# Optimization experiments

Hardware: AMD Instinct MI355X
Metric: run time of the kernel (lower is better)

## Reference

```python
import jax, jax.numpy as jnp
import numpy as np

B, T, D = 2, 2048, 1024
F = 4096
E = 8


def setup_inputs() -> dict:
    key = jax.random.key(0)
    k0, k1, k2, k3 = jax.random.split(key, 4)
    x = jax.random.normal(k0, (B, T, D), dtype=jnp.float32)
    Wg = jax.random.normal(k1, (E, D), dtype=jnp.float32) * 0.02   # gate Linear weight [E, D]
    W1 = jax.random.normal(k2, (E, D, F), dtype=jnp.float32) * 0.02  # expert up-proj
    W2 = jax.random.normal(k3, (E, F, D), dtype=jnp.float32) * 0.02  # expert down-proj
    return {"x": x, "Wg": Wg, "W1": W1, "W2": W2}


def reference(x, Wg, W1, W2):
    b, t, d = x.shape
    h = x.reshape(-1, d)                              # [N, D], N = b*t
    # --- top-2 gate ---
    logits = h @ Wg.T                                 # [N, E]
    scores, idx = jax.lax.top_k(logits, 2)            # [N, 2], [N, 2]
    scores = jax.nn.softmax(scores.astype(jnp.float32), axis=-1).astype(x.dtype)
    # --- all-expert dense FFN (SiLU MLP) ---
    up = jnp.einsum('nd,edf->enf', h, W1)             # [E, N, F]
    act = jax.nn.silu(up)
    out = jnp.einsum('enf,efd->ned', act, W2)         # [N, E, D]
    # --- combine top-2 ---
    sel = jnp.take_along_axis(out, idx[:, :, None], axis=1)  # [N, 2, D]
    y = jnp.sum(scores[:, :, None] * sel, axis=1)     # [N, D]
    return y.reshape(b, t, d)
```

## Files before the change

### kernel.cpp

```cpp
#include <hip/hip_runtime.h>
#include <hip/hip_bf16.h>
#include <stdint.h>

#define N_TOK 4096
#define D_DIM 1024
#define F_DIM 4096
#define E_NUM 8

typedef unsigned short u16;
typedef __attribute__((ext_vector_type(8))) short short8;
typedef __attribute__((ext_vector_type(4))) float f32x4;

__device__ __forceinline__ u16 f2bf(float f) {
  union { float f; uint32_t u; } v; v.f = f;
  uint32_t u = v.u;
  uint32_t r = (u + 0x7FFFu + ((u >> 16) & 1u)) >> 16;
  return (u16)r;
}

__device__ __forceinline__ void gld_lds16(const u16* g, u16* l) {
  __builtin_amdgcn_global_load_lds(
      (const __attribute__((address_space(1))) uint32_t*)g,
      (__attribute__((address_space(3))) uint32_t*)l, 16, 0, 0);
}

__global__ __launch_bounds__(256) void prep_kernel(
    const float* __restrict__ x, const float* __restrict__ Wg,
    const float* __restrict__ W1,
    u16* __restrict__ xb, int2* __restrict__ choice, float* __restrict__ sc2,
    u16* __restrict__ w1t) {
  int bid = blockIdx.x;
  if (bid < 1024) {
    int n = bid * 4 + (threadIdx.x >> 6);
    int l = threadIdx.x & 63;
    const float* xr = x + (size_t)n * D_DIM;
    u16* xbr = xb + (size_t)n * D_DIM;
    float acc[E_NUM];
#pragma unroll
    for (int e = 0; e < E_NUM; ++e) acc[e] = 0.f;
    for (int d = l; d < D_DIM; d += 64) {
      float xv = xr[d];
      xbr[d] = f2bf(xv);
#pragma unroll
      for (int e = 0; e < E_NUM; ++e) acc[e] += xv * Wg[e * D_DIM + d];
    }
#pragma unroll
    for (int e = 0; e < E_NUM; ++e) {
      float v = acc[e];
#pragma unroll
      for (int off = 32; off > 0; off >>= 1) v += __shfl_xor(v, off);
      acc[e] = v;
    }
    if (l == 0) {
      int i0 = 0; float m0 = acc[0];
#pragma unroll
      for (int e = 1; e < E_NUM; ++e) if (acc[e] > m0) { m0 = acc[e]; i0 = e; }
      int i1 = -1; float m1 = -INFINITY;
#pragma unroll
      for (int e = 0; e < E_NUM; ++e) if (e != i0 && acc[e] > m1) { m1 = acc[e]; i1 = e; }
      float z = __expf(m1 - m0);
      float s0 = 1.f / (1.f + z);
      sc2[n * 2 + 0] = s0;
      sc2[n * 2 + 1] = 1.f - s0;
      choice[n] = make_int2(i0, i1);
    }
    return;
  }
  __shared__ u16 tile[64][72];
  int s = bid - 1024;
  int bx = s & 63, by = (s >> 6) & 15, e = s >> 10;
  const int R = D_DIM, C = F_DIM;
  const float* src = W1 + (size_t)e * R * C;
  u16* dst = w1t + (size_t)e * R * C;
  int r0 = by * 64, c0 = bx * 64;
  int tid = threadIdx.x;
  int lr = tid & 15;
  int rr = tid >> 4;
#pragma unroll
  for (int p = 0; p < 4; ++p) {
    int r = rr + p * 16;
    float4 v = *(const float4*)&src[(size_t)(r0 + r) * C + c0 + lr * 4];
    tile[lr * 4 + 0][r] = f2bf(v.x);
    tile[lr * 4 + 1][r] = f2bf(v.y);
    tile[lr * 4 + 2][r] = f2bf(v.z);
    tile[lr * 4 + 3][r] = f2bf(v.w);
  }
  __syncthreads();
#pragma unroll
  for (int p = 0; p < 4; ++p) {
    int c = rr + p * 16;
    ushort4 o = *(const ushort4*)&tile[c][lr * 4];
    *(ushort4*)&dst[(size_t)(c0 + c) * R + r0 + lr * 4] = o;
  }
}

__global__ void route_kernel(const int2* __restrict__ choice, int* __restrict__ cnt,
                             int* __restrict__ tok_list) {
  int e = blockIdx.x;
  int l = threadIdx.x;
  unsigned long long below = (l == 0) ? 0ull : ((~0ull) >> (64 - l));
  int c = 0;
  for (int it = 0; it < N_TOK / 64; ++it) {
    int n = it * 64 + l;
    int2 ch = choice[n];
    unsigned long long b0 = __ballot(ch.x == e);
    if (ch.x == e) tok_list[e * N_TOK + c + __popcll(b0 & below)] = 2 * n;
    c += __popcll(b0);
    unsigned long long b1 = __ballot(ch.y == e);
    if (ch.y == e) tok_list[e * N_TOK + c + __popcll(b1 & below)] = 2 * n + 1;
    c += __popcll(b1);
  }
  if (l == 0) cnt[e] = c;
}

__global__ void prefix_kernel(const int* __restrict__ cnt, int* __restrict__ base) {
  if (threadIdx.x == 0) {
    int s = 0;
    for (int e = 0; e < E_NUM; ++e) { base[e] = s; s += cnt[e]; }
  }
}

__global__ __launch_bounds__(512) void up_gemm(
    const u16* __restrict__ xb, const u16* __restrict__ w1t,
    const float* __restrict__ W2, u16* __restrict__ w2t,
    const int* __restrict__ cnt, const int* __restrict__ base,
    const int* __restrict__ tok_list, u16* __restrict__ act) {
  __shared__ u16 smem[16384];

  const int bid = blockIdx.x;
  if (bid < 4096) {
    u16 (*tile)[72] = (u16(*)[72])smem;
    int s = bid;
    int bx = s & 7, by = (s >> 3) & 63, e = s >> 9;
    const int R = F_DIM, C = D_DIM;
    const float* src = W2 + (size_t)e * R * C;
    u16* dst = w2t + (size_t)e * R * C;
    int r0 = by * 64, c0 = bx * 128;
    int tid = threadIdx.x;
    {
      int sc = tid & 31, sr = tid >> 5;
      const float* b0p = &src[(size_t)(r0 + sr * 4) * C + c0 + sc * 4];
      float4 v0 = *(const float4*)(b0p + 0 * C);
      float4 v1 = *(const float4*)(b0p + 1 * C);
      float4 v2 = *(const float4*)(b0p + 2 * C);
      float4 v3 = *(const float4*)(b0p + 3 * C);
      ushort4 w;
      w.x = f2bf(v0.x); w.y = f2bf(v1.x); w.z = f2bf(v2.x); w.w = f2bf(v3.x);
      *(ushort4*)&tile[sc * 4 + 0][sr * 4] = w;
      w.x = f2bf(v0.y); w.y = f2bf(v1.y); w.z = f2bf(v2.y); w.w = f2bf(v3.y);
      *(ushort4*)&tile[sc * 4 + 1][sr * 4] = w;
      w.x = f2bf(v0.z); w.y = f2bf(v1.z); w.z = f2bf(v2.z); w.w = f2bf(v3.z);
      *(ushort4*)&tile[sc * 4 + 2][sr * 4] = w;
      w.x = f2bf(v0.w); w.y = f2bf(v1.w); w.z = f2bf(v2.w); w.w = f2bf(v3.w);
      *(ushort4*)&tile[sc * 4 + 3][sr * 4] = w;
    }
    __syncthreads();
    {
      int c = tid >> 2, rq = tid & 3;
      u16* dp = &dst[(size_t)(c0 + c) * R + r0 + rq * 16];
      const u16* tp = &tile[c][rq * 16];
      uint4 a0 = *(const uint4*)(tp + 0);
      uint4 a1 = *(const uint4*)(tp + 8);
      *(uint4*)(dp + 0) = a0;
      *(uint4*)(dp + 8) = a1;
    }
    return;
  }

  u16 (*As)[4096] = (u16(*)[4096])smem;
  u16 (*Bs)[4096] = (u16(*)[4096])(smem + 8192);

  const int ubid = bid - 4096;
  const int orig = (ubid & 7) * 1024 + (ubid >> 3);
  const int bx = orig & 31, by = (orig >> 5) & 31, e = orig >> 10;

  const int ce = cnt[e];
  const int row0 = by * 128;
  if (row0 >= ce) return;
  const int col0 = bx * 128;
  const int be = base[e];

  const int tid = threadIdx.x;
  const int wave = tid >> 6, lane = tid & 63;
  const int wm = wave >> 2, wn = wave & 3;
  const int lr = lane & 15, kq = lane >> 4;

  const int rsA = wave * 16 + (lane >> 2);
  const int kb = (((lane & 3) ^ ((lane >> 3) & 3)) * 8);
  const int kq8 = ((kq ^ ((lr >> 1) & 3)) * 8);

  int ga = row0 + rsA;
  int e0 = (ga < ce) ? (tok_list[e * N_TOK + ga] & (2 * N_TOK - 1)) : 0;
  const u16* srcA = xb + (e0 >> 1) * D_DIM + kb;
  const u16* srcB = w1t + (size_t)(e * F_DIM + col0 + rsA) * D_DIM + kb;

  f32x4 acc[4][2];
#pragma unroll
  for (int m = 0; m < 4; ++m)
#pragma unroll
    for (int n = 0; n < 2; ++n) acc[m][n] = (f32x4){0.f, 0.f, 0.f, 0.f};

#define USTAGE(k0, b)                              \
  do {                                             \
    gld_lds16(srcA + (k0), &As[b][wave * 512]);    \
    gld_lds16(srcB + (k0), &Bs[b][wave * 512]);    \
  } while (0)

#define UCOMPUTE(b)                                                           \
  do {                                                                        \
    short8 a[4], bb[2];                                                       \
    _Pragma("unroll") for (int m = 0; m < 4; ++m)                             \
        a[m] = *(const short8*)&As[b][(wm * 64 + m * 16 + lr) * 32 + kq8];    \
    _Pragma("unroll") for (int n = 0; n < 2; ++n)                             \
        bb[n] = *(const short8*)&Bs[b][(wn * 32 + n * 16 + lr) * 32 + kq8];   \
    _Pragma("unroll") for (int m = 0; m < 4; ++m)                             \
        _Pragma("unroll") for (int n = 0; n < 2; ++n)                         \
            acc[m][n] = __builtin_amdgcn_mfma_f32_16x16x32_bf16(a[m], bb[n], acc[m][n], 0, 0, 0); \
  } while (0)

  const int NT = D_DIM / 32;
  USTAGE(0, 0);
  USTAGE(32, 1);
  asm volatile("s_waitcnt vmcnt(2)" ::: "memory");
  __builtin_amdgcn_s_barrier();
  __builtin_amdgcn_sched_barrier(0);
  int cur = 0;
  for (int t = 0; t < NT; ++t) {
    UCOMPUTE(cur);
    __builtin_amdgcn_sched_barrier(0);
    __builtin_amdgcn_s_barrier();
    __builtin_amdgcn_sched_barrier(0);
    if (t + 2 < NT) {
      USTAGE((t + 2) * 32, cur);
      asm volatile("s_waitcnt vmcnt(2)" ::: "memory");
    } else {
      asm volatile("s_waitcnt vmcnt(0)" ::: "memory");
    }
    __builtin_amdgcn_s_barrier();
    __builtin_amdgcn_sched_barrier(0);
    cur ^= 1;
  }
#undef USTAGE
#undef UCOMPUTE

#pragma unroll
  for (int m = 0; m < 4; ++m) {
#pragma unroll
    for (int rg = 0; rg < 4; ++rg) {
      int row = wm * 64 + m * 16 + kq * 4 + rg;
      int i = row0 + row;
      if (i < ce) {
        u16* dst = act + (size_t)(be + i) * F_DIM + col0 + wn * 32;
#pragma unroll
        for (int n = 0; n < 2; ++n) {
          float v = acc[m][n][rg];
          float s = v / (1.f + __expf(-v));
          dst[n * 16 + lr] = f2bf(s);
        }
      }
    }
  }
}

__global__ __launch_bounds__(512) void down_gemm(
    const u16* __restrict__ act, const u16* __restrict__ w2t,
    const int* __restrict__ cnt, const int* __restrict__ base,
    const int* __restrict__ tok_list, const float* __restrict__ sc2,
    float* __restrict__ out) {
  __shared__ u16 As[2][128 * 32];
  __shared__ u16 Bs[2][128 * 32];
  __shared__ int toks[128];

  const int bid = blockIdx.x;
  const int orig = (bid & 7) * 256 + (bid >> 3);
  const int bx = orig & 7, by = (orig >> 3) & 31, e = orig >> 8;

  const int ce = cnt[e];
  const int row0 = by * 128;
  if (row0 >= ce) return;
  const int col0 = bx * 128;
  const int be = base[e];

  const int tid = threadIdx.x;
  const int wave = tid >> 6, lane = tid & 63;
  const int wm = wave >> 2, wn = wave & 3;
  const int lr = lane & 15, kq = lane >> 4;

  if (tid < 128) {
    int i = row0 + tid;
    toks[tid] = (i < ce) ? tok_list[e * N_TOK + i] : -1;
  }
  __syncthreads();

  const int rsA = wave * 16 + (lane >> 2);
  const int kb = (((lane & 3) ^ ((lane >> 3) & 3)) * 8);
  const int kq8 = ((kq ^ ((lr >> 1) & 3)) * 8);

  int ra = min(be + row0 + rsA, 2 * N_TOK - 1);
  const u16* srcA = act + (size_t)ra * F_DIM + kb;
  const u16* srcB = w2t + (size_t)(e * D_DIM + col0 + rsA) * F_DIM + kb;

  f32x4 acc[4][2];
#pragma unroll
  for (int m = 0; m < 4; ++m)
#pragma unroll
    for (int n = 0; n < 2; ++n) acc[m][n] = (f32x4){0.f, 0.f, 0.f, 0.f};

#define DSTAGE(k0, b)                              \
  do {                                             \
    gld_lds16(srcA + (k0), &As[b][wave * 512]);    \
    gld_lds16(srcB + (k0), &Bs[b][wave * 512]);    \
  } while (0)

#define DCOMPUTE(b)                                                           \
  do {                                                                        \
    short8 a[4], bb[2];                                                       \
    _Pragma("unroll") for (int m = 0; m < 4; ++m)                             \
        a[m] = *(const short8*)&As[b][(wm * 64 + m * 16 + lr) * 32 + kq8];    \
    _Pragma("unroll") for (int n = 0; n < 2; ++n)                             \
        bb[n] = *(const short8*)&Bs[b][(wn * 32 + n * 16 + lr) * 32 + kq8];   \
    _Pragma("unroll") for (int m = 0; m < 4; ++m)                             \
        _Pragma("unroll") for (int n = 0; n < 2; ++n)                         \
            acc[m][n] = __builtin_amdgcn_mfma_f32_16x16x32_bf16(a[m], bb[n], acc[m][n], 0, 0, 0); \
  } while (0)

  const int NT = F_DIM / 32;
  DSTAGE(0, 0);
  DSTAGE(32, 1);
  asm volatile("s_waitcnt vmcnt(2)" ::: "memory");
  __builtin_amdgcn_s_barrier();
  __builtin_amdgcn_sched_barrier(0);
  int cur = 0;
  for (int t = 0; t < NT; ++t) {
    DCOMPUTE(cur);
    __builtin_amdgcn_sched_barrier(0);
    __builtin_amdgcn_s_barrier();
    __builtin_amdgcn_sched_barrier(0);
    if (t + 2 < NT) {
      DSTAGE((t + 2) * 32, cur);
      asm volatile("s_waitcnt vmcnt(2)" ::: "memory");
    } else {
      asm volatile("s_waitcnt vmcnt(0)" ::: "memory");
    }
    __builtin_amdgcn_s_barrier();
    __builtin_amdgcn_sched_barrier(0);
    cur ^= 1;
  }
#undef DSTAGE
#undef DCOMPUTE

#pragma unroll
  for (int m = 0; m < 4; ++m) {
#pragma unroll
    for (int rg = 0; rg < 4; ++rg) {
      int row = wm * 64 + m * 16 + kq * 4 + rg;
      int ent = toks[row];
      if (ent >= 0) {
        int tokn = ent >> 1;
        float sc = sc2[tokn * 2 + (ent & 1)];
        float* dst = out + (size_t)tokn * D_DIM + col0 + wn * 32;
#pragma unroll
        for (int n = 0; n < 2; ++n)
          atomicAdd(&dst[n * 16 + lr], acc[m][n][rg] * sc);
      }
    }
  }
}

extern "C" void kernel_launch(void* const* d_in, const int* in_sizes, int n_in,
                              void* d_out, int out_size, void* d_ws, size_t ws_size,
                              hipStream_t stream) {
  const float* x  = (const float*)d_in[0];
  const float* Wg = (const float*)d_in[1];
  const float* W1 = (const float*)d_in[2];
  const float* W2 = (const float*)d_in[3];
  float* out = (float*)d_out;

  char* ws = (char*)d_ws;
  size_t off = 0;
  u16* xb  = (u16*)(ws + off); off += (size_t)N_TOK * D_DIM * 2;
  u16* w1t = (u16*)(ws + off); off += (size_t)E_NUM * F_DIM * D_DIM * 2;
  u16* w2t = (u16*)(ws + off); off += (size_t)E_NUM * D_DIM * F_DIM * 2;
  u16* act = (u16*)(ws + off); off += (size_t)2 * N_TOK * F_DIM * 2;
  int* tok_list = (int*)(ws + off); off += (size_t)E_NUM * N_TOK * 4;
  float* sc2 = (float*)(ws + off); off += (size_t)N_TOK * 2 * 4;
  int2* choice = (int2*)(ws + off); off += (size_t)N_TOK * 8;
  int* cnt  = (int*)(ws + off); off += 128;
  int* base = (int*)(ws + off); off += 128;

  hipMemsetAsync(d_out, 0, (size_t)out_size * 4, stream);

  prep_kernel<<<dim3(1024 + 8192), 256, 0, stream>>>(x, Wg, W1, xb, choice,
                                                     sc2, w1t);
  route_kernel<<<E_NUM, 64, 0, stream>>>(choice, cnt, tok_list);
  prefix_kernel<<<1, 1, 0, stream>>>(cnt, base);

  up_gemm<<<dim3(4096 + 8192), 512, 0, stream>>>(xb, w1t, W2, w2t, cnt, base,
                                                 tok_list, act);
  down_gemm<<<dim3(2048), 512, 0, stream>>>(act, w2t, cnt, base, tok_list, sc2, out);
}
```

Baseline: 314.7 us.

## Interleave W2 transpose blocks with up-GEMM blocks and inline expert base prefix

Removes the single-thread prefix kernel by computing each expert's base offset inline from the counts inside both GEMMs. Reorders up_gemm's grid so every third block performs a W2 transpose tile, interleaving memory-bound transpose work with compute-bound GEMM tiles instead of running all transpose blocks first. This aims to cut one launch and improve overlap across CUs. It may disturb the GEMM block swizzle's cache locality and adds an integer division per block.

New measurement: 320.8 us. No clear change (+1.9%).

```diff
diff --git a/kernel.cpp b/kernel.cpp
--- a/kernel.cpp
+++ b/kernel.cpp
@@ -113,24 +113,24 @@
   if (l == 0) cnt[e] = c;
 }
 
-__global__ void prefix_kernel(const int* __restrict__ cnt, int* __restrict__ base) {
-  if (threadIdx.x == 0) {
-    int s = 0;
-    for (int e = 0; e < E_NUM; ++e) { base[e] = s; s += cnt[e]; }
-  }
+__device__ __forceinline__ int inline_base(const int* cnt, int e) {
+  int b = 0;
+#pragma unroll
+  for (int j = 0; j < E_NUM; ++j) b += (j < e) ? cnt[j] : 0;
+  return b;
 }
 
 __global__ __launch_bounds__(512) void up_gemm(
     const u16* __restrict__ xb, const u16* __restrict__ w1t,
     const float* __restrict__ W2, u16* __restrict__ w2t,
-    const int* __restrict__ cnt, const int* __restrict__ base,
-    const int* __restrict__ tok_list, u16* __restrict__ act) {
+    const int* __restrict__ cnt, const int* __restrict__ tok_list,
+    u16* __restrict__ act) {
   __shared__ u16 smem[16384];
 
   const int bid = blockIdx.x;
-  if (bid < 4096) {
+  if (bid % 3 == 0) {
     u16 (*tile)[72] = (u16(*)[72])smem;
-    int s = bid;
+    int s = bid / 3;
     int bx = s & 7, by = (s >> 3) & 63, e = s >> 9;
     const int R = F_DIM, C = D_DIM;
     const float* src = W2 + (size_t)e * R * C;
@@ -170,7 +170,7 @@
   u16 (*As)[4096] = (u16(*)[4096])smem;
   u16 (*Bs)[4096] = (u16(*)[4096])(smem + 8192);
 
-  const int ubid = bid - 4096;
+  const int ubid = bid - bid / 3 - 1;
   const int orig = (ubid & 7) * 1024 + (ubid >> 3);
   const int bx = orig & 31, by = (orig >> 5) & 31, e = orig >> 10;
 
@@ -178,7 +178,7 @@
   const int row0 = by * 128;
   if (row0 >= ce) return;
   const int col0 = bx * 128;
-  const int be = base[e];
+  const int be = inline_base(cnt, e);
 
   const int tid = threadIdx.x;
   const int wave = tid >> 6, lane = tid & 63;
@@ -264,9 +264,8 @@
 
 __global__ __launch_bounds__(512) void down_gemm(
     const u16* __restrict__ act, const u16* __restrict__ w2t,
-    const int* __restrict__ cnt, const int* __restrict__ base,
-    const int* __restrict__ tok_list, const float* __restrict__ sc2,
-    float* __restrict__ out) {
+    const int* __restrict__ cnt, const int* __restrict__ tok_list,
+    const float* __restrict__ sc2, float* __restrict__ out) {
   __shared__ u16 As[2][128 * 32];
   __shared__ u16 Bs[2][128 * 32];
   __shared__ int toks[128];
@@ -279,7 +278,7 @@
   const int row0 = by * 128;
   if (row0 >= ce) return;
   const int col0 = bx * 128;
-  const int be = base[e];
+  const int be = inline_base(cnt, e);
 
   const int tid = threadIdx.x;
   const int wave = tid >> 6, lane = tid & 63;
@@ -386,16 +385,13 @@
   float* sc2 = (float*)(ws + off); off += (size_t)N_TOK * 2 * 4;
   int2* choice = (int2*)(ws + off); off += (size_t)N_TOK * 8;
   int* cnt  = (int*)(ws + off); off += 128;
-  int* base = (int*)(ws + off); off += 128;
 
   hipMemsetAsync(d_out, 0, (size_t)out_size * 4, stream);
 
   prep_kernel<<<dim3(1024 + 8192), 256, 0, stream>>>(x, Wg, W1, xb, choice,
                                                      sc2, w1t);
   route_kernel<<<E_NUM, 64, 0, stream>>>(choice, cnt, tok_list);
-  prefix_kernel<<<1, 1, 0, stream>>>(cnt, base);
-
-  up_gemm<<<dim3(4096 + 8192), 512, 0, stream>>>(xb, w1t, W2, w2t, cnt, base,
-                                                 tok_list, act);
-  down_gemm<<<dim3(2048), 512, 0, stream>>>(act, w2t, cnt, base, tok_list, sc2, out);
-}
+
+  up_gemm<<<dim3(12288), 512, 0, stream>>>(xb, w1t, W2, w2t, cnt, tok_list, act);
+  down_gemm<<<dim3(2048), 512, 0, stream>>>(act, w2t, cnt, tok_list, sc2, out);
+}
```
